# Optimization experiments

Measured on AMD Instinct MI355X. Metric: run time of the kernel, lower is better.

Reference implementation:

```python
import jax, jax.numpy as jnp
import numpy as np

D = 1024      # model dim
H = 16        # heads
DH = D // H   # head dim
T = 1024      # input tokens
B = 2         # batch
P = 4         # persistent tokens
WIN = 256     # sliding window
MH = 4 * D    # neural-memory hidden dim
FF = 4 * D    # ffn hidden dim
EPS = 1e-5


def _layernorm(x, g, b):
    m = jnp.mean(x, axis=-1, keepdims=True)
    v = jnp.mean((x - m) ** 2, axis=-1, keepdims=True)
    return (x - m) * jax.lax.rsqrt(v + EPS) * g + b


def setup_inputs() -> dict:
    key = jax.random.key(0)
    ks = jax.random.split(key, 12)
    s = 0.02
    return {
        "x": jax.random.normal(ks[0], (B, T, D), dtype=jnp.float32),
        "pmem": jax.random.normal(ks[1], (P, D), dtype=jnp.float32) * s,
        # neural memory MLP: dim -> MH -> dim (torch Linear convention W:(out,in))
        "mW1": jax.random.normal(ks[2], (MH, D), dtype=jnp.float32) * s,
        "mb1": jnp.zeros((MH,), dtype=jnp.float32),
        "mW2": jax.random.normal(ks[3], (D, MH), dtype=jnp.float32) * s,
        "mb2": jnp.zeros((D,), dtype=jnp.float32),
        "ln1_g": jnp.ones((D,), dtype=jnp.float32),
        "ln1_b": jnp.zeros((D,), dtype=jnp.float32),
        # MHA packed qkv in-proj and out-proj
        "Wqkv": jax.random.normal(ks[4], (3 * D, D), dtype=jnp.float32) * s,
        "bqkv": jnp.zeros((3 * D,), dtype=jnp.float32),
        "Wo": jax.random.normal(ks[5], (D, D), dtype=jnp.float32) * s,
        "bo": jnp.zeros((D,), dtype=jnp.float32),
        "ln2_g": jnp.ones((D,), dtype=jnp.float32),
        "ln2_b": jnp.zeros((D,), dtype=jnp.float32),
        "fW1": jax.random.normal(ks[6], (FF, D), dtype=jnp.float32) * s,
        "fb1": jnp.zeros((FF,), dtype=jnp.float32),
        "fW2": jax.random.normal(ks[7], (D, FF), dtype=jnp.float32) * s,
        "fb2": jnp.zeros((D,), dtype=jnp.float32),
    }


def _forward(x, pmem, mW1, mb1, mW2, mb2, ln1_g, ln1_b, Wqkv, bqkv, Wo, bo,
             ln2_g, ln2_b, fW1, fb1, fW2, fb2):
    Bc, Tc, Dc = x.shape
    # 1. retrieve from neural long-term memory: 2-layer MLP on x
    mem_ctx = jax.nn.relu(jnp.einsum('btd,hd->bth', x, mW1) + mb1)
    mem_ctx = jnp.einsum('bth,dh->btd', mem_ctx, mW2) + mb2
    # 2. concat persistent tokens, retrieved memory, x along sequence
    pers = jnp.broadcast_to(pmem[None], (Bc, P, Dc))
    aug = jnp.concatenate([pers, mem_ctx, x], axis=1)      # (B, L, D)
    L = aug.shape[1]
    # 3. sliding-window causal attention on norm1(aug)
    h = _layernorm(aug, ln1_g, ln1_b)
    qkv = jnp.einsum('bld,ed->ble', h, Wqkv) + bqkv        # (B, L, 3D)
    q, k, v = jnp.split(qkv, 3, axis=-1)
    q = q.reshape(Bc, L, H, DH)
    k = k.reshape(Bc, L, H, DH)
    v = v.reshape(Bc, L, H, DH)
    scale = 1.0 / np.sqrt(DH).astype(np.float32)
    scores = jnp.einsum('bqhd,bkhd->bhqk', q, k) * scale   # (B, H, L, L)
    i = jnp.arange(L)[:, None]
    j = jnp.arange(L)[None, :]
    allowed = (j <= i) & (j > i - WIN)                     # causal sliding window
    scores = jnp.where(allowed[None, None], scores, jnp.float32(-1e30))
    attn = jax.nn.softmax(scores, axis=-1)
    ctx = jnp.einsum('bhqk,bkhd->bqhd', attn, v).reshape(Bc, L, D)
    h_attn = jnp.einsum('bld,ed->ble', ctx, Wo) + bo
    # 4. residual + FFN
    h_res = aug + h_attn
    f = _layernorm(h_res, ln2_g, ln2_b)
    f = jax.nn.gelu(jnp.einsum('bld,fd->blf', f, fW1) + fb1, approximate=False)
    f = jnp.einsum('blf,df->bld', f, fW2) + fb2
    return h_res + f                                       # (B, P+2T, D)


def reference(x, pmem, mW1, mb1, mW2, mb2, ln1_g, ln1_b, Wqkv, bqkv, Wo, bo,
              ln2_g, ln2_b, fW1, fb1, fW2, fb2):
    return _forward(x, pmem, mW1, mb1, mW2, mb2, ln1_g, ln1_b, Wqkv, bqkv,
                    Wo, bo, ln2_g, ln2_b, fW1, fb1, fW2, fb2)
```

## Files before the change

### kernel.cpp

```cpp
#include <hip/hip_runtime.h>
#include <math.h>

#define D_   1024
#define H_   16
#define DH_  64
#define T_   1024
#define B_   2
#define P_   4
#define L_   2052
#define WIN_ 256
#define MH_  4096
#define FF_  4096

typedef __attribute__((ext_vector_type(8))) short bf16x8;
typedef __attribute__((ext_vector_type(4))) float f32x4;
typedef __attribute__((ext_vector_type(8))) unsigned short ush8;

__device__ __forceinline__ unsigned short f2bf(float f) {
  unsigned int u = __builtin_bit_cast(unsigned int, f);
  u += 0x7fffu + ((u >> 16) & 1u);
  return (unsigned short)(u >> 16);
}
__device__ __forceinline__ float bf2f(unsigned short h) {
  unsigned int u = ((unsigned int)h) << 16;
  return __builtin_bit_cast(float, u);
}

__device__ __forceinline__ void gl16(const unsigned short* g, unsigned short* l) {
  __builtin_amdgcn_global_load_lds(
      (const __attribute__((address_space(1))) unsigned int*)g,
      (__attribute__((address_space(3))) unsigned int*)l, 16, 0, 0);
}

__global__ void cvt_bf16_k(const float* __restrict__ in, unsigned short* __restrict__ out, int n) {
  int i = blockIdx.x * blockDim.x + threadIdx.x;
  int e = i * 4;
  if (e >= n) return;
  float4 v = *(const float4*)(in + e);
  ushort4 o;
  o.x = f2bf(v.x); o.y = f2bf(v.y); o.z = f2bf(v.z); o.w = f2bf(v.w);
  *(ushort4*)(out + e) = o;
}

__global__ void concat_k(const float* __restrict__ x, const float* __restrict__ pmem,
                         const float* __restrict__ p0, const float* __restrict__ p1,
                         const float* __restrict__ mb2, float* __restrict__ aug) {
  int i = blockIdx.x * blockDim.x + threadIdx.x;
  if (i >= (B_ * L_ * D_) / 4) return;
  int e = i * 4;
  int d  = e % D_;
  int rl = (e / D_) % L_;
  int b  = e / (D_ * L_);
  float4 v;
  if (rl < P_) {
    v = *(const float4*)(pmem + rl * D_ + d);
  } else if (rl < P_ + T_) {
    size_t idx = (size_t)(b * T_ + (rl - P_)) * D_ + d;
    float4 a0 = *(const float4*)(p0 + idx);
    float4 a1 = *(const float4*)(p1 + idx);
    float4 bb = *(const float4*)(mb2 + d);
    v = make_float4(a0.x + a1.x + bb.x, a0.y + a1.y + bb.y,
                    a0.z + a1.z + bb.z, a0.w + a1.w + bb.w);
  } else {
    v = *(const float4*)(x + (size_t)(b * T_ + (rl - P_ - T_)) * D_ + d);
  }
  *(float4*)(aug + e) = v;
}

__global__ void reduce10_k(const float* __restrict__ p0, const float* __restrict__ p1,
                           const float* __restrict__ hres, const float* __restrict__ fb2,
                           float* __restrict__ out) {
  int i = blockIdx.x * blockDim.x + threadIdx.x;
  if (i >= (B_ * L_ * D_) / 4) return;
  int e = i * 4;
  int d = e % D_;
  float4 a0 = *(const float4*)(p0 + e);
  float4 a1 = *(const float4*)(p1 + e);
  float4 hr = *(const float4*)(hres + e);
  float4 bb = *(const float4*)(fb2 + d);
  float4 v = make_float4(a0.x + a1.x + hr.x + bb.x, a0.y + a1.y + hr.y + bb.y,
                         a0.z + a1.z + hr.z + bb.z, a0.w + a1.w + hr.w + bb.w);
  *(float4*)(out + e) = v;
}

__global__ __launch_bounds__(256)
void layernorm_k(const float* __restrict__ in, const float* __restrict__ g,
                 const float* __restrict__ bb, unsigned short* __restrict__ out) {
  const int row = blockIdx.x;
  const int tid = threadIdx.x;
  const float* xr = in + (size_t)row * D_;
  float4 v = *(const float4*)(xr + tid * 4);
  float s  = v.x + v.y + v.z + v.w;
  float sq = v.x * v.x + v.y * v.y + v.z * v.z + v.w * v.w;
  #pragma unroll
  for (int o = 1; o < 64; o <<= 1) { s += __shfl_xor(s, o); sq += __shfl_xor(sq, o); }
  __shared__ float red[8];
  const int wid = tid >> 6;
  if ((tid & 63) == 0) { red[wid] = s; red[4 + wid] = sq; }
  __syncthreads();
  s  = red[0] + red[1] + red[2] + red[3];
  sq = red[4] + red[5] + red[6] + red[7];
  const float mean = s * (1.0f / D_);
  const float var  = sq * (1.0f / D_) - mean * mean;
  const float inv  = rsqrtf(var + 1e-5f);
  const int c = tid * 4;
  float4 gv = *(const float4*)(g + c);
  float4 bv = *(const float4*)(bb + c);
  unsigned short* dst = out + (size_t)row * D_ + c;
  dst[0] = f2bf((v.x - mean) * inv * gv.x + bv.x);
  dst[1] = f2bf((v.y - mean) * inv * gv.y + bv.y);
  dst[2] = f2bf((v.z - mean) * inv * gv.z + bv.z);
  dst[3] = f2bf((v.w - mean) * inv * gv.w + bv.w);
}

template<int ACT, int OUTBF, int RESID, int WM, int WN, int NWR, int NWC, int KS, int PART>
__global__ __launch_bounds__(KS * NWR * NWC * 64)
void gemm_bt_k(const unsigned short* __restrict__ A,
               const unsigned short* __restrict__ W,
               const float* __restrict__ bias,
               const float* __restrict__ resid,
               void* __restrict__ Cv,
               int M, int N, int K, int ldK, long long zstride) {
  constexpr int NW = NWR * NWC;
  constexpr int BM = NWR * WM * 16;
  constexpr int BN = NWC * WN * 16;
  constexpr int STG = 2 * KS * (BM + BN) * 32 * 2;
  constexpr int RED = (KS > 1) ? BM * BN * 4 : 0;
  constexpr int SBYTES = STG > RED ? STG : RED;
  __shared__ __align__(16) char smem[SBYTES];
  unsigned short* sA = (unsigned short*)smem;
  unsigned short* sB = sA + 2 * KS * BM * 32;

  const int tid  = threadIdx.x;
  const int lane = tid & 63;
  const int wv   = tid >> 6;
  const int grp  = wv / NW;
  const int wg   = wv % NW;
  const int wr   = wg / NWC, wc = wg % NWC;
  const int gm0  = blockIdx.y * BM;
  const int gn0  = blockIdx.x * BN;
  const int KperG = K / KS;
  const int NT    = KperG / 32;
  const int zofs  = PART ? blockIdx.z * K : 0;

  const f32x4 fz = {0.f, 0.f, 0.f, 0.f};
  f32x4 acc[WM][WN];
  #pragma unroll
  for (int i = 0; i < WM; ++i)
    #pragma unroll
    for (int j = 0; j < WN; ++j) acc[i][j] = fz;

  const int srow = lane >> 2;
  const int skc  = (lane & 3) * 8;
  const unsigned short* gA = A + (size_t)(gm0 + srow) * ldK + grp * KperG + zofs + skc;
  const unsigned short* gB = W + (size_t)(gn0 + srow) * ldK + grp * KperG + zofs + skc;

  const int fr = lane & 15;
  const int fk = (lane >> 4) * 8;

  auto stage = [&](int d, int k0) {
    unsigned short* dA = sA + (d * KS + grp) * BM * 32;
    unsigned short* dB = sB + (d * KS + grp) * BN * 32;
    #pragma unroll
    for (int t = 0; t < BM / (NW * 16); ++t) {
      const int rr = wg * 16 + t * NW * 16;
      gl16(gA + (size_t)rr * ldK + k0, dA + rr * 32);
    }
    #pragma unroll
    for (int t = 0; t < BN / (NW * 16); ++t) {
      const int rr = wg * 16 + t * NW * 16;
      gl16(gB + (size_t)rr * ldK + k0, dB + rr * 32);
    }
  };

  stage(0, 0);
  for (int kt = 0; kt < NT; ++kt) {
    __syncthreads();
    if (kt + 1 < NT) stage((kt + 1) & 1, (kt + 1) * 32);
    const int d = kt & 1;
    const unsigned short* lA = sA + (d * KS + grp) * BM * 32;
    const unsigned short* lB = sB + (d * KS + grp) * BN * 32;
    bf16x8 af[WM], bfr[WN];
    #pragma unroll
    for (int i = 0; i < WM; ++i) af[i]  = *(const bf16x8*)&lA[(wr * WM * 16 + i * 16 + fr) * 32 + fk];
    #pragma unroll
    for (int j = 0; j < WN; ++j) bfr[j] = *(const bf16x8*)&lB[(wc * WN * 16 + j * 16 + fr) * 32 + fk];
    #pragma unroll
    for (int i = 0; i < WM; ++i)
      #pragma unroll
      for (int j = 0; j < WN; ++j)
        acc[i][j] = __builtin_amdgcn_mfma_f32_16x16x32_bf16(af[i], bfr[j], acc[i][j], 0, 0, 0);
  }

  if (KS > 1) {
    __syncthreads();
    f32x4* sR = (f32x4*)smem;
    const int tg = tid & (NW * 64 - 1);
    for (int g = 1; g < KS; ++g) {
      if (grp == g) {
        #pragma unroll
        for (int i = 0; i < WM; ++i)
          #pragma unroll
          for (int j = 0; j < WN; ++j) sR[(tg * WM + i) * WN + j] = acc[i][j];
      }
      __syncthreads();
      if (grp == 0) {
        #pragma unroll
        for (int i = 0; i < WM; ++i)
          #pragma unroll
          for (int j = 0; j < WN; ++j) {
            f32x4 t = sR[(tg * WM + i) * WN + j];
            #pragma unroll
            for (int r = 0; r < 4; ++r) acc[i][j][r] += t[r];
          }
      }
      __syncthreads();
    }
    if (grp != 0) return;
  }

  const int rq = (lane >> 4) * 4;
  if (PART) {
    float* Pout = (float*)Cv + (size_t)blockIdx.z * zstride;
    #pragma unroll
    for (int i = 0; i < WM; ++i) {
      #pragma unroll
      for (int j = 0; j < WN; ++j) {
        const int col = gn0 + wc * WN * 16 + j * 16 + fr;
        #pragma unroll
        for (int r = 0; r < 4; ++r) {
          const int row = gm0 + wr * WM * 16 + i * 16 + rq + r;
          if (row < M) Pout[(size_t)row * N + col] = acc[i][j][r];
        }
      }
    }
    return;
  }
  #pragma unroll
  for (int i = 0; i < WM; ++i) {
    #pragma unroll
    for (int j = 0; j < WN; ++j) {
      const int col = gn0 + wc * WN * 16 + j * 16 + fr;
      const float bcol = bias[col];
      #pragma unroll
      for (int r = 0; r < 4; ++r) {
        const int row = gm0 + wr * WM * 16 + i * 16 + rq + r;
        if (row < M) {
          float v = acc[i][j][r] + bcol;
          if (RESID) v += resid[(size_t)row * N + col];
          if (ACT == 1) v = fmaxf(v, 0.f);
          if (ACT == 2) v = 0.5f * v * (1.0f + erff(v * 0.70710678f));
          if (OUTBF) ((unsigned short*)Cv)[(size_t)row * N + col] = f2bf(v);
          else       ((float*)Cv)[(size_t)row * N + col] = v;
        }
      }
    }
  }
}

__global__ __launch_bounds__(256)
void attn_k(const float* __restrict__ qkv, unsigned short* __restrict__ ctx) {
  __shared__ unsigned short Kb[64][72];
  __shared__ unsigned short Vt[64][72];
  __shared__ unsigned short Ps[4][16][72];
  const int tid  = threadIdx.x;
  const int lane = tid & 63;
  const int w    = tid >> 6;
  const int l15  = lane & 15;
  const int l4   = lane >> 4;
  const int qb   = blockIdx.x * 64;
  const int h    = blockIdx.y;
  const int b    = blockIdx.z;

  int qrow = qb + w * 16 + l15;
  if (qrow >= L_) qrow = L_ - 1;
  const float* qp = qkv + ((size_t)(b * L_ + qrow)) * 3072 + h * 64;
  bf16x8 aq0, aq1;
  #pragma unroll
  for (int e = 0; e < 8; ++e) {
    aq0[e] = (short)f2bf(qp[l4 * 8 + e] * 0.125f);
    aq1[e] = (short)f2bf(qp[32 + l4 * 8 + e] * 0.125f);
  }

  const f32x4 fz = {0.f, 0.f, 0.f, 0.f};
  f32x4 acc_o[4];
  #pragma unroll
  for (int j = 0; j < 4; ++j) acc_o[j] = fz;
  float m_[4], ls[4];
  #pragma unroll
  for (int r = 0; r < 4; ++r) { m_[r] = -3.0e38f; ls[r] = 0.f; }

  int k0 = qb - WIN_;
  if (k0 < 0) k0 = 0;

  for (int kb = k0; kb <= qb; kb += 64) {
    #pragma unroll
    for (int c = tid; c < 1024; c += 256) {
      const int row = c >> 4;
      const int cc  = (c & 15) * 4;
      const int g   = kb + row;
      float4 kv = make_float4(0.f, 0.f, 0.f, 0.f), vv = kv;
      if (g < L_) {
        const float* base = qkv + ((size_t)(b * L_ + g)) * 3072 + h * 64 + cc;
        kv = *(const float4*)(base + 1024);
        vv = *(const float4*)(base + 2048);
      }
      ushort4 k4; k4.x = f2bf(kv.x); k4.y = f2bf(kv.y); k4.z = f2bf(kv.z); k4.w = f2bf(kv.w);
      *(ushort4*)&Kb[row][cc] = k4;
      Vt[cc + 0][row] = f2bf(vv.x);
      Vt[cc + 1][row] = f2bf(vv.y);
      Vt[cc + 2][row] = f2bf(vv.z);
      Vt[cc + 3][row] = f2bf(vv.w);
    }
    __syncthreads();

    f32x4 s[4];
    #pragma unroll
    for (int kt = 0; kt < 4; ++kt) {
      bf16x8 bk0 = *(const bf16x8*)&Kb[kt * 16 + l15][l4 * 8];
      bf16x8 bk1 = *(const bf16x8*)&Kb[kt * 16 + l15][32 + l4 * 8];
      f32x4 t = __builtin_amdgcn_mfma_f32_16x16x32_bf16(aq0, bk0, fz, 0, 0, 0);
      s[kt]   = __builtin_amdgcn_mfma_f32_16x16x32_bf16(aq1, bk1, t,  0, 0, 0);
    }

    #pragma unroll
    for (int r = 0; r < 4; ++r) {
      const int qg = qb + w * 16 + l4 * 4 + r;
      float rm = -3.0e38f;
      #pragma unroll
      for (int kt = 0; kt < 4; ++kt) {
        const int kg = kb + kt * 16 + l15;
        const bool ok = (kg <= qg) && (kg + WIN_ > qg);
        rm = fmaxf(rm, ok ? s[kt][r] : -3.0e38f);
      }
      rm = fmaxf(rm, __shfl_xor(rm, 1));
      rm = fmaxf(rm, __shfl_xor(rm, 2));
      rm = fmaxf(rm, __shfl_xor(rm, 4));
      rm = fmaxf(rm, __shfl_xor(rm, 8));
      const float mn = fmaxf(m_[r], rm);
      const float sf = __expf(m_[r] - mn);
      m_[r] = mn;
      float ps = 0.f;
      #pragma unroll
      for (int kt = 0; kt < 4; ++kt) {
        const int kg = kb + kt * 16 + l15;
        const bool ok = (kg <= qg) && (kg + WIN_ > qg);
        const float p = ok ? __expf(s[kt][r] - mn) : 0.f;
        ps += p;
        Ps[w][l4 * 4 + r][kt * 16 + l15] = f2bf(p);
      }
      ps += __shfl_xor(ps, 1);
      ps += __shfl_xor(ps, 2);
      ps += __shfl_xor(ps, 4);
      ps += __shfl_xor(ps, 8);
      ls[r] = ls[r] * sf + ps;
      #pragma unroll
      for (int j = 0; j < 4; ++j) acc_o[j][r] *= sf;
    }

    #pragma unroll
    for (int ks = 0; ks < 2; ++ks) {
      bf16x8 pa = *(const bf16x8*)&Ps[w][l15][ks * 32 + l4 * 8];
      #pragma unroll
      for (int j = 0; j < 4; ++j) {
        bf16x8 vb = *(const bf16x8*)&Vt[j * 16 + l15][ks * 32 + l4 * 8];
        acc_o[j] = __builtin_amdgcn_mfma_f32_16x16x32_bf16(pa, vb, acc_o[j], 0, 0, 0);
      }
    }
    __syncthreads();
  }

  #pragma unroll
  for (int r = 0; r < 4; ++r) {
    const int qg = qb + w * 16 + l4 * 4 + r;
    if (qg < L_) {
      const float inv = 1.0f / ls[r];
      unsigned short* dst = ctx + ((size_t)(b * L_ + qg)) * 1024 + h * 64 + l15;
      #pragma unroll
      for (int j = 0; j < 4; ++j) dst[j * 16] = f2bf(acc_o[j][r] * inv);
    }
  }
}

extern "C" void kernel_launch(void* const* d_in, const int* in_sizes, int n_in,
                              void* d_out, int out_size, void* d_ws, size_t ws_size,
                              hipStream_t stream) {
  (void)in_sizes; (void)n_in; (void)out_size; (void)ws_size;
  const float* x    = (const float*)d_in[0];
  const float* pmem = (const float*)d_in[1];
  const float* mW1  = (const float*)d_in[2];
  const float* mb1  = (const float*)d_in[3];
  const float* mW2  = (const float*)d_in[4];
  const float* mb2  = (const float*)d_in[5];
  const float* ln1g = (const float*)d_in[6];
  const float* ln1b = (const float*)d_in[7];
  const float* Wqkv = (const float*)d_in[8];
  const float* bqkv = (const float*)d_in[9];
  const float* Wo   = (const float*)d_in[10];
  const float* bo   = (const float*)d_in[11];
  const float* ln2g = (const float*)d_in[12];
  const float* ln2b = (const float*)d_in[13];
  const float* fW1  = (const float*)d_in[14];
  const float* fb1  = (const float*)d_in[15];
  const float* fW2  = (const float*)d_in[16];
  const float* fb2  = (const float*)d_in[17];
  float* outp = (float*)d_out;
  char* ws = (char*)d_ws;

  unsigned short* w1b   = (unsigned short*)(ws + 0ull);
  unsigned short* w2b   = (unsigned short*)(ws + 8388608ull);
  unsigned short* wqkvb = (unsigned short*)(ws + 16777216ull);
  unsigned short* wob   = (unsigned short*)(ws + 23068672ull);
  unsigned short* fw1b  = (unsigned short*)(ws + 25165824ull);
  unsigned short* fw2b  = (unsigned short*)(ws + 33554432ull);
  const size_t S = 41943040ull;
  float* aug  = (float*)(ws + S);
  float* hres = (float*)(ws + S + 16809984ull);
  unsigned short* hlnbuf = (unsigned short*)(ws + S + 33619968ull);
  char* R = ws + S + 42270720ull;
  unsigned short* xb   = (unsigned short*)(R);
  unsigned short* h1   = (unsigned short*)(R + 4194304ull);
  float* qkv           = (float*)(R);
  unsigned short* f1   = (unsigned short*)(R + 15826944ull);
  unsigned short* hln  = hlnbuf;
  unsigned short* ctxb = hlnbuf;
  unsigned short* hln2 = hlnbuf;
  float* g2p = hres;
  float* g10p = aug;
  const long long Z10 = 8404992LL;

  auto cvt = [&](const float* src, unsigned short* dst, int n) {
    cvt_bf16_k<<<dim3((n / 4 + 255) / 256), dim3(256), 0, stream>>>(src, dst, n);
  };
  cvt(x,    xb,    B_ * T_ * D_);
  cvt(mW1,  w1b,   MH_ * D_);
  cvt(mW2,  w2b,   D_ * MH_);
  cvt(Wqkv, wqkvb, 3 * D_ * D_);
  cvt(Wo,   wob,   D_ * D_);
  cvt(fW1,  fw1b,  FF_ * D_);
  cvt(fW2,  fw2b,  D_ * FF_);

  const int BT = B_ * T_;
  const int BL = B_ * L_;
  const int NE4 = B_ * L_ * D_ / 4;

  gemm_bt_k<1, 1, 0, 4, 4, 2, 2, 1, 0><<<dim3(MH_ / 128, BT / 128), 256, 0, stream>>>(xb, w1b, mb1, nullptr, h1, BT, MH_, D_, D_, 0);
  gemm_bt_k<0, 0, 0, 4, 4, 2, 2, 1, 1><<<dim3(D_ / 128, BT / 128, 2), 256, 0, stream>>>(h1, w2b, nullptr, nullptr, g2p, BT, D_, MH_ / 2, MH_, (long long)BT * D_);
  concat_k<<<dim3((NE4 + 255) / 256), 256, 0, stream>>>(x, pmem, g2p, g2p + (size_t)BT * D_, mb2, aug);
  layernorm_k<<<dim3(BL), 256, 0, stream>>>(aug, ln1g, ln1b, hln);
  gemm_bt_k<0, 0, 0, 4, 4, 2, 2, 1, 0><<<dim3(3 * D_ / 128, (BL + 127) / 128), 256, 0, stream>>>(hln, wqkvb, bqkv, nullptr, qkv, BL, 3 * D_, D_, D_, 0);
  attn_k<<<dim3((L_ + 63) / 64, H_, B_), 256, 0, stream>>>(qkv, ctxb);
  gemm_bt_k<0, 0, 1, 2, 4, 4, 1, 1, 0><<<dim3(D_ / 64, (BL + 127) / 128), 256, 0, stream>>>(ctxb, wob, bo, aug, hres, BL, D_, D_, D_, 0);
  layernorm_k<<<dim3(BL), 256, 0, stream>>>(hres, ln2g, ln2b, hln2);
  gemm_bt_k<2, 1, 0, 4, 4, 2, 2, 1, 0><<<dim3(FF_ / 128, (BL + 127) / 128), 256, 0, stream>>>(hln2, fw1b, fb1, nullptr, f1, BL, FF_, D_, D_, 0);
  gemm_bt_k<0, 0, 0, 4, 4, 2, 2, 1, 1><<<dim3(D_ / 128, (BL + 127) / 128, 2), 256, 0, stream>>>(f1, fw2b, nullptr, nullptr, g10p, BL, D_, FF_ / 2, FF_, Z10);
  reduce10_k<<<dim3((NE4 + 255) / 256), 256, 0, stream>>>(g10p, g10p + Z10, hres, fb2, outp);
}
```

Baseline: 373.4 us.

## Swizzle GEMM tiles across XCDs, store QKV as bf16, use tanh-approx GELU

Three unrelated changes. First, GEMM workgroup indices are remapped so that consecutive tiles land on the same XCD, which should improve L2 reuse on the multi-die MI355X. Second, the QKV projection now writes bf16 instead of fp32, which halves QKV write and attention read traffic and removes in-kernel conversions. Third, the exact erf GELU is replaced with a tanh approximation built on fast exp and fast division, which is cheaper but shifts numerics slightly away from the reference's exact GELU.

```diff
diff --git a/kernel.cpp b/kernel.cpp
--- a/kernel.cpp
+++ b/kernel.cpp
@@ -137,8 +137,16 @@
   const int grp  = wv / NW;
   const int wg   = wv % NW;
   const int wr   = wg / NWC, wc = wg % NWC;
-  const int gm0  = blockIdx.y * BM;
-  const int gn0  = blockIdx.x * BN;
+
+  const unsigned int gridX = gridDim.x;
+  const unsigned int flat  = blockIdx.y * gridX + blockIdx.x;
+  const unsigned int nwg   = gridX * gridDim.y;
+  const unsigned int q8 = nwg >> 3, r8 = nwg & 7;
+  const unsigned int xcd = flat & 7, sidx = flat >> 3;
+  const unsigned int swz = (xcd < r8 ? xcd * (q8 + 1) : r8 * (q8 + 1) + (xcd - r8) * q8) + sidx;
+  const int gm0 = (int)(swz / gridX) * BM;
+  const int gn0 = (int)(swz % gridX) * BN;
+
   const int KperG = K / KS;
   const int NT    = KperG / 32;
   const int zofs  = PART ? blockIdx.z * K : 0;
@@ -249,7 +257,11 @@
           float v = acc[i][j][r] + bcol;
           if (RESID) v += resid[(size_t)row * N + col];
           if (ACT == 1) v = fmaxf(v, 0.f);
-          if (ACT == 2) v = 0.5f * v * (1.0f + erff(v * 0.70710678f));
+          if (ACT == 2) {
+            float t = 0.7978845608f * v * (1.0f + 0.044715f * v * v);
+            float e = __expf(2.0f * t);
+            v = v - __fdividef(v, e + 1.0f);
+          }
           if (OUTBF) ((unsigned short*)Cv)[(size_t)row * N + col] = f2bf(v);
           else       ((float*)Cv)[(size_t)row * N + col] = v;
         }
@@ -259,7 +271,7 @@
 }
 
 __global__ __launch_bounds__(256)
-void attn_k(const float* __restrict__ qkv, unsigned short* __restrict__ ctx) {
+void attn_k(const unsigned short* __restrict__ qkv, unsigned short* __restrict__ ctx) {
   __shared__ unsigned short Kb[64][72];
   __shared__ unsigned short Vt[64][72];
   __shared__ unsigned short Ps[4][16][72];
@@ -274,12 +286,12 @@
 
   int qrow = qb + w * 16 + l15;
   if (qrow >= L_) qrow = L_ - 1;
-  const float* qp = qkv + ((size_t)(b * L_ + qrow)) * 3072 + h * 64;
+  const unsigned short* qp = qkv + ((size_t)(b * L_ + qrow)) * 3072 + h * 64;
   bf16x8 aq0, aq1;
   #pragma unroll
   for (int e = 0; e < 8; ++e) {
-    aq0[e] = (short)f2bf(qp[l4 * 8 + e] * 0.125f);
-    aq1[e] = (short)f2bf(qp[32 + l4 * 8 + e] * 0.125f);
+    aq0[e] = (short)f2bf(bf2f(qp[l4 * 8 + e]) * 0.125f);
+    aq1[e] = (short)f2bf(bf2f(qp[32 + l4 * 8 + e]) * 0.125f);
   }
 
   const f32x4 fz = {0.f, 0.f, 0.f, 0.f};
@@ -295,22 +307,19 @@
 
   for (int kb = k0; kb <= qb; kb += 64) {
     #pragma unroll
-    for (int c = tid; c < 1024; c += 256) {
-      const int row = c >> 4;
-      const int cc  = (c & 15) * 4;
+    for (int c = tid; c < 512; c += 256) {
+      const int row = c >> 3;
+      const int cc  = (c & 7) * 8;
       const int g   = kb + row;
-      float4 kv = make_float4(0.f, 0.f, 0.f, 0.f), vv = kv;
+      ush8 kv8 = {0, 0, 0, 0, 0, 0, 0, 0}, vv8 = kv8;
       if (g < L_) {
-        const float* base = qkv + ((size_t)(b * L_ + g)) * 3072 + h * 64 + cc;
-        kv = *(const float4*)(base + 1024);
-        vv = *(const float4*)(base + 2048);
-      }
-      ushort4 k4; k4.x = f2bf(kv.x); k4.y = f2bf(kv.y); k4.z = f2bf(kv.z); k4.w = f2bf(kv.w);
-      *(ushort4*)&Kb[row][cc] = k4;
-      Vt[cc + 0][row] = f2bf(vv.x);
-      Vt[cc + 1][row] = f2bf(vv.y);
-      Vt[cc + 2][row] = f2bf(vv.z);
-      Vt[cc + 3][row] = f2bf(vv.w);
+        const unsigned short* base = qkv + ((size_t)(b * L_ + g)) * 3072 + h * 64 + cc;
+        kv8 = *(const ush8*)(base + 1024);
+        vv8 = *(const ush8*)(base + 2048);
+      }
+      *(ush8*)&Kb[row][cc] = kv8;
+      #pragma unroll
+      for (int e = 0; e < 8; ++e) Vt[cc + e][row] = vv8[e];
     }
     __syncthreads();
 
@@ -420,7 +429,7 @@
   char* R = ws + S + 42270720ull;
   unsigned short* xb   = (unsigned short*)(R);
   unsigned short* h1   = (unsigned short*)(R + 4194304ull);
-  float* qkv           = (float*)(R);
+  unsigned short* qkvb = (unsigned short*)(R);
   unsigned short* f1   = (unsigned short*)(R + 15826944ull);
   unsigned short* hln  = hlnbuf;
   unsigned short* ctxb = hlnbuf;
@@ -448,8 +457,8 @@
   gemm_bt_k<0, 0, 0, 4, 4, 2, 2, 1, 1><<<dim3(D_ / 128, BT / 128, 2), 256, 0, stream>>>(h1, w2b, nullptr, nullptr, g2p, BT, D_, MH_ / 2, MH_, (long long)BT * D_);
   concat_k<<<dim3((NE4 + 255) / 256), 256, 0, stream>>>(x, pmem, g2p, g2p + (size_t)BT * D_, mb2, aug);
   layernorm_k<<<dim3(BL), 256, 0, stream>>>(aug, ln1g, ln1b, hln);
-  gemm_bt_k<0, 0, 0, 4, 4, 2, 2, 1, 0><<<dim3(3 * D_ / 128, (BL + 127) / 128), 256, 0, stream>>>(hln, wqkvb, bqkv, nullptr, qkv, BL, 3 * D_, D_, D_, 0);
-  attn_k<<<dim3((L_ + 63) / 64, H_, B_), 256, 0, stream>>>(qkv, ctxb);
+  gemm_bt_k<0, 1, 0, 4, 4, 2, 2, 1, 0><<<dim3(3 * D_ / 128, (BL + 127) / 128), 256, 0, stream>>>(hln, wqkvb, bqkv, nullptr, qkvb, BL, 3 * D_, D_, D_, 0);
+  attn_k<<<dim3((L_ + 63) / 64, H_, B_), 256, 0, stream>>>(qkvb, ctxb);
   gemm_bt_k<0, 0, 1, 2, 4, 4, 1, 1, 0><<<dim3(D_ / 64, (BL + 127) / 128), 256, 0, stream>>>(ctxb, wob, bo, aug, hres, BL, D_, D_, D_, 0);
   layernorm_k<<<dim3(BL), 256, 0, stream>>>(hres, ln2g, ln2b, hln2);
   gemm_bt_k<2, 1, 0, 4, 4, 2, 2, 1, 0><<<dim3(FF_ / 128, (BL + 127) / 128), 256, 0, stream>>>(hln2, fw1b, fb1, nullptr, f1, BL, FF_, D_, D_, 0);
```

New measurement: 362.6 us. -2.9%, faster.
